# Kernel tuning notes

Measured on AMD Instinct MI355X. Metric: run time of the kernel, lower is better.

The kernel has to match this reference:

```python
import jax, jax.numpy as jnp
import numpy as np

K = 32  # neighbors, from init kwarg k


def setup_inputs() -> dict:
    key = jax.random.key(0)
    k1, k2, k3, k4 = jax.random.split(key, 4)
    N_train, N_test, D = 32768, 4096, 64
    x_train = jax.random.normal(k1, (N_train, D), dtype=jnp.float32)
    y_train = jax.random.randint(k2, (N_train,), 0, 1000, dtype=jnp.int64)
    x_test = jax.random.normal(k3, (N_test, D), dtype=jnp.float32)
    w_train = jax.random.uniform(k4, (N_train,), dtype=jnp.float32)
    return {"x_train": x_train, "y_train": y_train, "x_test": x_test, "w_train": w_train}


def _cdist(a, b):
    # Euclidean distance matrix [Na, Nb], matching torch.cdist(p=2)
    a2 = jnp.sum(a * a, axis=-1, keepdims=True)          # [Na,1]
    b2 = jnp.sum(b * b, axis=-1)[None, :]                # [1,Nb]
    sq = a2 + b2 - 2.0 * (a @ b.T)
    return jnp.sqrt(jnp.maximum(sq, 0.0))


def reference(x_train, y_train, x_test, w_train):
    n_test = x_test.shape[0]
    n_train = x_train.shape[0]
    dists = _cdist(x_test, x_train)                      # [N_test, N_train]
    # k smallest distances -> negate and take top_k
    _, indices = jax.lax.top_k(-dists, K)                # [N_test, K]
    knn_labels = y_train[indices]                        # [N_test, K]
    knn_w = w_train[indices]                             # [N_test, K]
    # weighted scatter vote: vote_pool[j, y_train[i]] += w_train[i]
    rows = jnp.arange(n_test)[:, None]                   # [N_test, 1]
    vote_pool = jnp.zeros((n_test, n_train), dtype=jnp.float32)
    vote_pool = vote_pool.at[rows, knn_labels].add(knn_w)
    return jnp.argmax(vote_pool, axis=1)
```

## Files before the change

kernel.cpp:

```cpp
#include <hip/hip_runtime.h>

#define NTRAIN 32768
#define NTEST  4096
#define DIM    64
#define KSEL   32
#define NLAB   1000
#define NCH    16
#define CHCOLS 2048
#define SLOT   112
#define NBIN   256
#define SSAMP  8192
#define SRANK2 32
#define POOLCAP 1792
#define WCOEF  0.01f

using short8 = __attribute__((ext_vector_type(8))) short;
using f32x4  = __attribute__((ext_vector_type(4))) float;
typedef unsigned short u16;

__device__ __forceinline__ unsigned f2u(float f){
  unsigned b = __float_as_uint(f);
  return (b & 0x80000000u) ? ~b : (b | 0x80000000u);
}
__device__ __forceinline__ u16 f2b(float x){
  unsigned u = __float_as_uint(x);
  return (u16)((u + 0x7fffu + ((u >> 16) & 1u)) >> 16);
}

struct Sel {
  unsigned hist[2048];
  unsigned wsum[4];
  unsigned sB, sLess, sU;
  int sNeed;
};

__device__ unsigned radix_select(const unsigned* __restrict__ keys, int n,
                                 unsigned rank, Sel* s, int t, int* needOut)
{
  const int lane = t & 63, wid = t >> 6;
  unsigned target = rank, pref = 0;
  for (int lev = 0; lev < 3; ++lev){
    const int nb    = (lev == 2) ? 1024 : 2048;
    const int shift = (lev == 0) ? 21 : (lev == 1 ? 10 : 0);
    for (int q = t; q < nb; q += 256) s->hist[q] = 0;
    __syncthreads();
    for (int i = t; i < n; i += 256){
      unsigned u = keys[i];
      bool ok = (lev == 0) ? true
              : (lev == 1) ? ((u >> 21) == pref)
                           : ((u >> 10) == pref);
      if (ok) atomicAdd(&s->hist[(u >> shift) & (unsigned)(nb - 1)], 1u);
    }
    __syncthreads();
    const int g = nb / 256;
    unsigned sl = 0;
#pragma unroll
    for (int k = 0; k < 8; ++k) if (k < g) sl += s->hist[t*g + k];
    unsigned x = sl;
#pragma unroll
    for (int ofs = 1; ofs < 64; ofs <<= 1){
      unsigned v = __shfl_up(x, (unsigned)ofs, 64);
      if (lane >= ofs) x += v;
    }
    if (lane == 63) s->wsum[wid] = x;
    __syncthreads();
    unsigned woff = 0;
#pragma unroll
    for (int w = 0; w < 4; ++w) if (w < wid) woff += s->wsum[w];
    unsigned incl = x + woff;
    unsigned excl = incl - sl;
    if (excl < target && target <= incl){
      unsigned cum = excl; int b = t*g;
      while (cum + s->hist[b] < target){ cum += s->hist[b]; ++b; }
      s->sB = (unsigned)b; s->sLess = cum;
    }
    __syncthreads();
    unsigned B = s->sB, cl = s->sLess;
    target -= cl;
    if      (lev == 0) pref = B;
    else if (lev == 1) pref = (pref << 11) | B;
    else if (t == 0){ s->sU = (pref << 10) | B; s->sNeed = (int)target; }
  }
  __syncthreads();
  *needOut = s->sNeed;
  return s->sU;
}

__device__ void select32(const unsigned* ku, const unsigned* ki, int n,
                         Sel* s, unsigned* tieI, unsigned* selI,
                         int* selCnt, int* tieCnt, int t)
{
  int need;
  unsigned ustar = radix_select(ku, n, KSEL, s, t, &need);
  if (t == 0){ *selCnt = 0; *tieCnt = 0; }
  __syncthreads();
  for (int i = t; i < n; i += 256){
    unsigned u = ku[i];
    if (u < ustar){ int p = atomicAdd(selCnt, 1); if (p < 40) selI[p] = ki[i]; }
    else if (u == ustar){ int p = atomicAdd(tieCnt, 1); if (p < 256) tieI[p] = ki[i]; }
  }
  __syncthreads();
  int nT = *tieCnt; if (nT > 256) nT = 256;
  if (t < nT){
    unsigned my = tieI[t]; int r = 0;
    for (int k = 0; k < nT; ++k) r += (tieI[k] < my) ? 1 : 0;
    if (r < need){ int p = atomicAdd(selCnt, 1); if (p < 40) selI[p] = my; }
  }
  __syncthreads();
}

__global__ void calib(int* __restrict__ MT, int* __restrict__ JT,
                      int* __restrict__ okf)
{
  const int l = threadIdx.x;
  const int v = l & 15;
  short8 av, onev, kv;
  u16 vb  = f2b((float)(v + 1));
  u16 one = (u16)0x3F80;
#pragma unroll
  for (int e = 0; e < 8; ++e){
    ((u16*)&av)[e]   = vb;
    ((u16*)&onev)[e] = one;
    ((u16*)&kv)[e]   = f2b((float)((l >> 4)*8 + e + 1));
  }
  f32x4 dA = {0,0,0,0}, dB = {0,0,0,0}, dK = {0,0,0,0};
  dA = __builtin_amdgcn_mfma_f32_16x16x32_bf16(av, onev, dA, 0,0,0);
  dB = __builtin_amdgcn_mfma_f32_16x16x32_bf16(onev, av, dB, 0,0,0);
  dK = __builtin_amdgcn_mfma_f32_16x16x32_bf16(kv, kv, dK, 0,0,0);
  bool ok = true;
#pragma unroll
  for (int e = 0; e < 4; ++e){
    int mi = (int)(dA[e]*(1.0f/32.0f) + 0.5f) - 1;
    int ji = (int)(dB[e]*(1.0f/32.0f) + 0.5f) - 1;
    if (mi < 0 || mi > 15 || dA[e] != 32.0f*(float)(mi+1)) ok = false;
    if (ji < 0 || ji > 15 || dB[e] != 32.0f*(float)(ji+1)) ok = false;
    if (dK[e] != 11440.0f) ok = false;
    MT[l*4 + e] = mi & 15;
    JT[l*4 + e] = ji & 15;
  }
  unsigned long long bal = __ballot(ok);
  if (l == 0) okf[0] = (bal == ~0ull) ? 1 : 0;
}

__global__ __launch_bounds__(256) void prep(const float* __restrict__ xtr,
        u16* __restrict__ xtr16, float* __restrict__ hb2,
        float* __restrict__ stats)
{
  int j = blockIdx.x*256 + threadIdx.x;
  const float4* rp = (const float4*)(xtr + (size_t)j*DIM);
  u16* orow = xtr16 + (size_t)j*DIM;
  float s = 0.f;
#pragma unroll
  for (int q = 0; q < 16; ++q){
    float4 w = rp[q];
    uint2 pk;
    pk.x = (unsigned)f2b(w.x) | ((unsigned)f2b(w.y) << 16);
    pk.y = (unsigned)f2b(w.z) | ((unsigned)f2b(w.w) << 16);
    *(uint2*)(orow + q*4) = pk;
    s = fmaf(w.x,w.x,s); s = fmaf(w.y,w.y,s);
    s = fmaf(w.z,w.z,s); s = fmaf(w.w,w.w,s);
  }
  float hs = 0.5f * s;
  hb2[j] = hs;
  float r0 = hs, r1 = hs*hs, r2 = s;
#pragma unroll
  for (int msk = 1; msk < 64; msk <<= 1){
    r0 += __shfl_xor(r0, msk, 64);
    r1 += __shfl_xor(r1, msk, 64);
    r2 = fmaxf(r2, __shfl_xor(r2, msk, 64));
  }
  if ((threadIdx.x & 63) == 0){
    atomicAdd(&stats[0], r0);
    atomicAdd(&stats[1], r1);
    atomicMax((unsigned*)&stats[2], __float_as_uint(r2));
  }
}

__global__ __launch_bounds__(256) void prepT(const float* __restrict__ xtst,
        u16* __restrict__ xtst16, const float* __restrict__ stats,
        float* __restrict__ loT, float* __restrict__ bsT, float* __restrict__ Wt)
{
  int m = blockIdx.x*256 + threadIdx.x;
  const float4* rp = (const float4*)(xtst + (size_t)m*DIM);
  u16* orow = xtst16 + (size_t)m*DIM;
  float s = 0.f;
#pragma unroll
  for (int q = 0; q < 16; ++q){
    float4 w = rp[q];
    uint2 pk;
    pk.x = (unsigned)f2b(w.x) | ((unsigned)f2b(w.y) << 16);
    pk.y = (unsigned)f2b(w.z) | ((unsigned)f2b(w.w) << 16);
    *(uint2*)(orow + q*4) = pk;
    s = fmaf(w.x,w.x,s); s = fmaf(w.y,w.y,s);
    s = fmaf(w.z,w.z,s); s = fmaf(w.w,w.w,s);
  }
  const float invN = 1.0f/(float)NTRAIN;
  float C   = stats[0]*invN;
  float var = fmaxf(stats[1]*invN - C*C, 0.f);
  float mb  = __uint_as_float(*(const unsigned*)&stats[2]);
  float sig = sqrtf(var + s) + 1e-6f;
  loT[m] = C - 12.f*sig;
  bsT[m] = 16.f/sig;
  Wt[m]  = WCOEF * sqrtf(s * mb);
}

__global__ __launch_bounds__(256) void sampleT(const u16* __restrict__ xtr16,
        const u16* __restrict__ xtst16, const float* __restrict__ hb2,
        const float* __restrict__ loT, const float* __restrict__ bsT,
        const float* __restrict__ Wt, const int* __restrict__ MT,
        const int* __restrict__ JT, const int* __restrict__ okf,
        float* __restrict__ TfB, float* __restrict__ thrFB)
{
  __shared__ unsigned histL[16*NBIN];
  __shared__ float hbS[SSAMP];

  const int t = threadIdx.x, lane = t & 63, w = t >> 6;
  const int m0 = blockIdx.x * 16;
  if (okf[0] == 0){
    if (t < 16){ TfB[m0+t] = 0.f; thrFB[m0+t] = -3.0e38f; }
    return;
  }
  const int oprow = lane & 15, kgrp = lane >> 4;

  for (int i = t; i < 16*NBIN; i += 256) histL[i] = 0;
  for (int i = t; i < SSAMP; i += 256) hbS[i] = hb2[i];

  int Ml[4], Jl[4];
#pragma unroll
  for (int e = 0; e < 4; ++e){ Ml[e] = MT[lane*4+e]; Jl[e] = JT[lane*4+e]; }

  const u16* ap = xtst16 + (size_t)(m0 + oprow)*DIM + kgrp*8;
  short8 a00 = *(const short8*)ap;
  short8 a01 = *(const short8*)(ap + 32);

  float lo0[4], bs0[4];
#pragma unroll
  for (int e = 0; e < 4; ++e){
    lo0[e] = loT[m0 + Ml[e]]; bs0[e] = bsT[m0 + Ml[e]];
  }
  __syncthreads();

  const int wcol = w*(SSAMP/4);
  const u16* bp = xtr16 + (size_t)(wcol + oprow)*DIM + kgrp*8;

#pragma unroll 2
  for (int jt = 0; jt < SSAMP/64; ++jt){
    short8 b0 = *(const short8*)bp;
    short8 b1 = *(const short8*)(bp + 32);
    f32x4 c0 = {0.f,0.f,0.f,0.f};
    c0 = __builtin_amdgcn_mfma_f32_16x16x32_bf16(a00, b0, c0, 0,0,0);
    c0 = __builtin_amdgcn_mfma_f32_16x16x32_bf16(a01, b1, c0, 0,0,0);
    const int jl = wcol + jt*16;
#pragma unroll
    for (int e = 0; e < 4; ++e){
      float h = hbS[jl + Jl[e]];
      float f = (h - c0[e] - lo0[e]) * bs0[e];
      if (f < 161.f){
        int b = (f < 0.f) ? 0 : (int)f;
        atomicAdd(&histL[Ml[e]*NBIN + b], 1u);
      }
    }
    bp += 16*DIM;
  }
  __syncthreads();
  if (t < 16){
    const unsigned* h = &histL[t*NBIN];
    unsigned cum = 0; int b = -1;
    for (int i = 0; i <= 160; ++i){
      cum += h[i];
      if (cum >= SRANK2){ b = i; break; }
    }
    int m = m0 + t;
    if (b < 0){ TfB[m] = 0.f; thrFB[m] = -3.0e38f; }
    else {
      float Te = loT[m] + (float)(b + 1) / bsT[m];
      float Wv = Wt[m];
      TfB[m]   = Te + 1.5f*Wv;
      thrFB[m] = Te + 2.5f*Wv;
    }
  }
}

__global__ __launch_bounds__(256) void knnA(const u16* __restrict__ xtr16,
        const u16* __restrict__ xtst16, const float* __restrict__ hb2,
        const float* __restrict__ thrFB, const int* __restrict__ MT,
        const int* __restrict__ JT, const int* __restrict__ okf,
        unsigned* __restrict__ cnt2, u16* __restrict__ cand)
{
  __shared__ float hbS[CHCOLS];
  __shared__ u16 lbuf[32][SLOT];
  __shared__ unsigned lcnt[32];

  const int t = threadIdx.x, lane = t & 63, w = t >> 6;
  const int jc = blockIdx.x & (NCH-1), mg = blockIdx.x >> 4;
  const int m0 = mg*32, col0 = jc*CHCOLS;

  if (okf[0] == 0){
    if (t < 32) cnt2[(size_t)jc*NTEST + m0 + t] = 0xFFFFFFFFu;
    return;
  }
  const int oprow = lane & 15, kgrp = lane >> 4;

  if (t < 32) lcnt[t] = 0;
  for (int i = t; i < CHCOLS; i += 256) hbS[i] = hb2[col0 + i];

  int Ml[4], Jl[4];
#pragma unroll
  for (int e = 0; e < 4; ++e){ Ml[e] = MT[lane*4+e]; Jl[e] = JT[lane*4+e]; }

  const u16* ap = xtst16 + (size_t)(m0 + oprow)*DIM + kgrp*8;
  short8 a00 = *(const short8*)ap;
  short8 a01 = *(const short8*)(ap + 32);
  short8 a10 = *(const short8*)(ap + 16*DIM);
  short8 a11 = *(const short8*)(ap + 16*DIM + 32);

  float th0[4], th1[4];
#pragma unroll
  for (int e = 0; e < 4; ++e){
    th0[e] = thrFB[m0 + Ml[e]];
    th1[e] = thrFB[m0 + 16 + Ml[e]];
  }
  float tm0 = fmaxf(fmaxf(th0[0],th0[1]), fmaxf(th0[2],th0[3]));
  float tm1 = fmaxf(fmaxf(th1[0],th1[1]), fmaxf(th1[2],th1[3]));

  __syncthreads();

  const int wcol = w*(CHCOLS/4);
  const u16* bp = xtr16 + (size_t)(col0 + wcol + oprow)*DIM + kgrp*8;

#pragma unroll 2
  for (int jt = 0; jt < CHCOLS/64; ++jt){
    short8 b0 = *(const short8*)bp;
    short8 b1 = *(const short8*)(bp + 32);
    f32x4 c0 = {0.f,0.f,0.f,0.f}, c1 = {0.f,0.f,0.f,0.f};
    c0 = __builtin_amdgcn_mfma_f32_16x16x32_bf16(a00, b0, c0, 0,0,0);
    c0 = __builtin_amdgcn_mfma_f32_16x16x32_bf16(a01, b1, c0, 0,0,0);
    c1 = __builtin_amdgcn_mfma_f32_16x16x32_bf16(a10, b0, c1, 0,0,0);
    c1 = __builtin_amdgcn_mfma_f32_16x16x32_bf16(a11, b1, c1, 0,0,0);
    const int jl = wcol + jt*16;
    float h[4];
#pragma unroll
    for (int e = 0; e < 4; ++e) h[e] = hbS[jl + Jl[e]];
    float g0 = fmaxf(fmaxf(c0[0]-h[0], c0[1]-h[1]), fmaxf(c0[2]-h[2], c0[3]-h[3]));
    if (g0 + tm0 > 0.f){
#pragma unroll
      for (int e = 0; e < 4; ++e) if (h[e] - c0[e] < th0[e]){
        unsigned p = atomicAdd(&lcnt[Ml[e]], 1u);
        if (p < SLOT) lbuf[Ml[e]][p] = (u16)(jl + Jl[e]);
      }
    }
    float g1 = fmaxf(fmaxf(c1[0]-h[0], c1[1]-h[1]), fmaxf(c1[2]-h[2], c1[3]-h[3]));
    if (g1 + tm1 > 0.f){
#pragma unroll
      for (int e = 0; e < 4; ++e) if (h[e] - c1[e] < th1[e]){
        unsigned p = atomicAdd(&lcnt[16 + Ml[e]], 1u);
        if (p < SLOT) lbuf[16 + Ml[e]][p] = (u16)(jl + Jl[e]);
      }
    }
    bp += 16*DIM;
  }
  __syncthreads();
  if (t < 32) cnt2[(size_t)jc*NTEST + m0 + t] = lcnt[t];
  const unsigned* lb32 = (const unsigned*)lbuf;
  unsigned* c32 = (unsigned*)cand;
  for (int i = t; i < 32*(SLOT/2); i += 256){
    int ms = i / (SLOT/2), e = i - ms*(SLOT/2);
    c32[((size_t)(m0 + ms)*NCH + jc)*(SLOT/2) + e] = lb32[i];
  }
}

__global__ __launch_bounds__(256) void knnB(const float* __restrict__ x_train,
        const float* __restrict__ hb2, const float* __restrict__ x_test,
        const int* __restrict__ y_train, const float* __restrict__ w_train,
        const float* __restrict__ TfB, const int* __restrict__ okf,
        const unsigned* __restrict__ cnt2, const u16* __restrict__ cand,
        int* __restrict__ out)
{
  __shared__ unsigned ku[POOLCAP], ki[POOLCAP];
  __shared__ unsigned chunkKeys[1024];
  __shared__ Sel ss;
  __shared__ unsigned tieI[256];
  __shared__ unsigned selI[40];
  __shared__ unsigned selR[KSEL];
  __shared__ int selCnt, tieCnt, poolCnt, nBelow, badJ;
  __shared__ float votes[NLAB];
  __shared__ unsigned cntS[NCH];
  __shared__ int yv[KSEL]; __shared__ float wv[KSEL];

  const int t = threadIdx.x, m = blockIdx.x;
  float a[DIM];
  const float4* am = (const float4*)(x_test + (size_t)m*DIM);
#pragma unroll
  for (int q = 0; q < 16; ++q){
    float4 v = am[q];
    a[4*q]=v.x; a[4*q+1]=v.y; a[4*q+2]=v.z; a[4*q+3]=v.w;
  }
  if (t < NCH) cntS[t] = cnt2[(size_t)t*NTEST + m];
  if (t == 0){ nBelow = 0; badJ = 0; }
  __syncthreads();

  bool ovf = (okf[0] == 0);
  unsigned offs[NCH+1]; offs[0] = 0;
#pragma unroll
  for (int jcc = 0; jcc < NCH; ++jcc){
    unsigned cc = cntS[jcc];
    if (cc > SLOT) ovf = true;
    offs[jcc+1] = offs[jcc] + ((cc > SLOT) ? SLOT : cc);
  }
  int c = (int)offs[NCH];
  bool mainok = !ovf && c >= KSEL;

  if (mainok){
#pragma unroll
    for (int jcc = 0; jcc < NCH; ++jcc){
      unsigned cc = cntS[jcc];
      for (unsigned i = t; i < cc; i += 256){
        unsigned v = cand[((size_t)m*NCH + jcc)*SLOT + i];
        if (v >= CHCOLS){ badJ = 1; v = 0; }
        ki[offs[jcc] + i] = (unsigned)(jcc*CHCOLS) + v;
      }
    }
    __syncthreads();
    if (badJ) mainok = false;
  }
  const float Tf = TfB[m];
  if (mainok){
    for (int i = t; i < c; i += 256){
      unsigned j = ki[i];
      const float4* rp = (const float4*)(x_train + (size_t)j*DIM);
      float s = 0.f;
#pragma unroll
      for (int q = 0; q < 16; ++q){
        float4 v = rp[q];
        s = fmaf(a[4*q],v.x,s); s = fmaf(a[4*q+1],v.y,s);
        s = fmaf(a[4*q+2],v.z,s); s = fmaf(a[4*q+3],v.w,s);
      }
      float kf = hb2[j] - s;
      ku[i] = f2u(kf);
      if (kf < Tf) atomicAdd(&nBelow, 1);
    }
    __syncthreads();
    mainok = (nBelow >= KSEL);
  }

  if (mainok){
    select32(ku, ki, c, &ss, tieI, selI, &selCnt, &tieCnt, t);
    if (t < KSEL) selR[t] = selI[t];
    __syncthreads();
  } else {
    if (t == 0) poolCnt = 0;
    __syncthreads();
    for (int ch = 0; ch < NTRAIN/1024; ++ch){
      const int j0 = ch*1024;
      for (int q = 0; q < 4; ++q){
        int j = j0 + q*256 + t;
        const float4* rp = (const float4*)(x_train + (size_t)j*DIM);
        float s = 0.f;
#pragma unroll
        for (int qq = 0; qq < 16; ++qq){
          float4 v = rp[qq];
          s = fmaf(a[4*qq],v.x,s); s = fmaf(a[4*qq+1],v.y,s);
          s = fmaf(a[4*qq+2],v.z,s); s = fmaf(a[4*qq+3],v.w,s);
        }
        chunkKeys[q*256 + t] = f2u(hb2[j] - s);
      }
      __syncthreads();
      int need;
      unsigned ustar = radix_select(chunkKeys, 1024, KSEL, &ss, t, &need);
      for (int q = 0; q < 4; ++q){
        unsigned u = chunkKeys[q*256 + t];
        if (u <= ustar){
          int p = atomicAdd(&poolCnt, 1);
          if (p < POOLCAP){ ku[p] = u; ki[p] = (unsigned)(j0 + q*256 + t); }
        }
      }
      __syncthreads();
    }
    int n = poolCnt; if (n > POOLCAP) n = POOLCAP;
    select32(ku, ki, n, &ss, tieI, selI, &selCnt, &tieCnt, t);
    if (t < KSEL) selR[t] = selI[t];
    __syncthreads();
  }

  for (int q = t; q < NLAB; q += 256) votes[q] = 0.f;
  if (t < KSEL){
    unsigned my = selR[t]; int r = 0;
#pragma unroll
    for (int k = 0; k < KSEL; ++k) r += (selR[k] < my) ? 1 : 0;
    yv[r] = y_train[my]; wv[r] = w_train[my];
  }
  __syncthreads();
  if (t == 0){
    for (int r = 0; r < KSEL; ++r) votes[yv[r]] += wv[r];
  }
  __syncthreads();

  float* rv = (float*)ss.hist;
  int*   rl = (int*)(ss.hist + 256);
  float bv = -1.f; int bl = 0;
  for (int l = t; l < NLAB; l += 256){
    float v = votes[l];
    if (v > bv){ bv = v; bl = l; }
  }
  rv[t] = bv; rl[t] = bl;
  __syncthreads();
  for (int sred = 128; sred > 0; sred >>= 1){
    if (t < sred){
      if (rv[t+sred] > rv[t] || (rv[t+sred] == rv[t] && rl[t+sred] < rl[t])){
        rv[t] = rv[t+sred]; rl[t] = rl[t+sred];
      }
    }
    __syncthreads();
  }
  if (t == 0) out[m] = rl[0];
}

__global__ __launch_bounds__(256) void knn_legacy(
    const float* __restrict__ x_train, const float* __restrict__ x_test,
    const int* __restrict__ y_train, const float* __restrict__ w_train,
    int* __restrict__ out)
{
  __shared__ unsigned keys[16384];
  __shared__ Sel ss;
  __shared__ unsigned candU[64];
  __shared__ unsigned candI[64];
  __shared__ unsigned tieI[256];
  __shared__ int nCand, nTie;
  __shared__ float rv[256]; __shared__ int rl[256];

  float* votes = (float*)ss.hist;
  const int t = threadIdx.x;
  const int m = blockIdx.x;

  float a[DIM];
  const float* am = x_test + (size_t)m * DIM;
#pragma unroll
  for (int d = 0; d < DIM; ++d) a[d] = am[d];

  if (t == 0) nCand = 0;

  for (int h = 0; h < 2; ++h){
    __syncthreads();
    for (int i = 0; i < 64; ++i){
      int j = h*16384 + i*256 + t;
      const float4* bp = (const float4*)(x_train + (size_t)j * DIM);
      float s = 0.f;
#pragma unroll
      for (int q = 0; q < 16; ++q){
        float4 v = bp[q];
        float e0 = a[4*q]   - v.x, e1 = a[4*q+1] - v.y;
        float e2 = a[4*q+2] - v.z, e3 = a[4*q+3] - v.w;
        s = fmaf(e0,e0,s); s = fmaf(e1,e1,s); s = fmaf(e2,e2,s); s = fmaf(e3,e3,s);
      }
      keys[i*256 + t] = f2u(s);
    }
    __syncthreads();

    int need;
    unsigned ustar = radix_select(keys, 16384, KSEL, &ss, t, &need);
    if (t == 0) nTie = 0;
    __syncthreads();

    for (int i = 0; i < 64; ++i){
      unsigned u   = keys[i*256 + t];
      unsigned idx = (unsigned)(h*16384 + i*256 + t);
      if (u < ustar){
        int p = atomicAdd(&nCand, 1);
        if (p < 64){ candU[p] = u; candI[p] = idx; }
      } else if (u == ustar){
        int p = atomicAdd(&nTie, 1);
        if (p < 256) tieI[p] = idx;
      }
    }
    __syncthreads();
    int nT = nTie; if (nT > 256) nT = 256;
    if (t < nT){
      unsigned my = tieI[t]; int r = 0;
      for (int k = 0; k < nT; ++k) r += (tieI[k] < my) ? 1 : 0;
      if (r < need){
        int p = atomicAdd(&nCand, 1);
        if (p < 64){ candU[p] = ustar; candI[p] = my; }
      }
    }
    __syncthreads();
  }

  for (int q = t; q < NLAB; q += 256) votes[q] = 0.f;
  __syncthreads();
  int nC = nCand; if (nC > 64) nC = 64;
  if (t < nC){
    unsigned mu = candU[t], mi = candI[t];
    int r = 0;
    for (int k = 0; k < nC; ++k){
      unsigned kku = candU[k], kki = candI[k];
      r += (kku < mu || (kku == mu && kki < mi)) ? 1 : 0;
    }
    if (r < KSEL){
      int lab = y_train[mi];
      atomicAdd(&votes[lab], w_train[mi]);
    }
  }
  __syncthreads();

  float bv = -1.f; int bl = 0;
  for (int l = t; l < NLAB; l += 256){
    float v = votes[l];
    if (v > bv){ bv = v; bl = l; }
  }
  rv[t] = bv; rl[t] = bl;
  __syncthreads();
  for (int s = 128; s > 0; s >>= 1){
    if (t < s){
      if (rv[t+s] > rv[t] || (rv[t+s] == rv[t] && rl[t+s] < rl[t])){
        rv[t] = rv[t+s]; rl[t] = rl[t+s];
      }
    }
    __syncthreads();
  }
  if (t == 0) out[m] = rl[0];
}

extern "C" void kernel_launch(void* const* d_in, const int* in_sizes, int n_in,
                              void* d_out, int out_size, void* d_ws, size_t ws_size,
                              hipStream_t stream)
{
  (void)in_sizes; (void)n_in; (void)out_size;
  const float* x_train = (const float*)d_in[0];
  const int*   y_train = (const int*)  d_in[1];
  const float* x_test  = (const float*)d_in[2];
  const float* w_train = (const float*)d_in[3];
  int* out = (int*)d_out;

  char* p = (char*)d_ws;
  u16*      xtr16  = (u16*)p;      p += (size_t)NTRAIN*DIM*2;
  u16*      xtst16 = (u16*)p;      p += (size_t)NTEST*DIM*2;
  float*    hb2    = (float*)p;    p += (size_t)NTRAIN*4;
  float*    loT    = (float*)p;    p += (size_t)NTEST*4;
  float*    bsT    = (float*)p;    p += (size_t)NTEST*4;
  float*    Wt     = (float*)p;    p += (size_t)NTEST*4;
  float*    TfB    = (float*)p;    p += (size_t)NTEST*4;
  float*    thrFB  = (float*)p;    p += (size_t)NTEST*4;
  unsigned* cnt2   = (unsigned*)p; p += (size_t)NCH*NTEST*4;
  int*      MT     = (int*)p;      p += 64*4*4;
  int*      JT     = (int*)p;      p += 64*4*4;
  int*      okf    = (int*)p;      p += 256;
  float*    stats  = (float*)p;    p += 512;
  u16*      cand   = (u16*)p;      p += (size_t)NTEST*NCH*SLOT*2;
  size_t need = (size_t)(p - (char*)d_ws);

  if (ws_size >= need){
    hipMemsetAsync(stats, 0, 512, stream);
    calib<<<1, 64, 0, stream>>>(MT, JT, okf);
    prep <<<NTRAIN/256, 256, 0, stream>>>(x_train, xtr16, hb2, stats);
    prepT<<<NTEST/256,  256, 0, stream>>>(x_test, xtst16, stats, loT, bsT, Wt);
    sampleT<<<NTEST/16, 256, 0, stream>>>(xtr16, xtst16, hb2, loT, bsT, Wt,
                                          MT, JT, okf, TfB, thrFB);
    knnA<<<(NTEST/32)*NCH, 256, 0, stream>>>(xtr16, xtst16, hb2, thrFB,
                                             MT, JT, okf, cnt2, cand);
    knnB<<<NTEST, 256, 0, stream>>>(x_train, hb2, x_test, y_train, w_train,
                                    TfB, okf, cnt2, cand, out);
  } else {
    knn_legacy<<<NTEST, 256, 0, stream>>>(x_train, x_test, y_train, w_train, out);
  }
}
```

Baseline: 304.3 us.

## Split threshold sampling across blocks, compact knnB candidates and shrink shared memory

The sampleT histogram pass is split into two half-sample blocks per row group. Each block merges its local histogram into a global histogram with atomics, and a new scanT kernel derives the thresholds from it. In knnB, only candidates below the threshold are compacted into a small buffer and ranked directly, which replaces the general radix select32 on the main path. Shared arrays are overlaid in a union to cut LDS use, and the final argmax uses wave shuffles instead of a shared-memory tree. The cost is an extra kernel launch, a memset, global atomics, and an O(n²) rank step that depends on how many candidates fall below the threshold.

```diff
diff --git a/kernel.cpp b/kernel.cpp
--- a/kernel.cpp
+++ b/kernel.cpp
@@ -10,7 +10,9 @@
 #define SLOT   112
 #define NBIN   256
 #define SSAMP  8192
+#define SHALF  (SSAMP/2)
 #define SRANK2 32
+#define SCAP   512
 #define POOLCAP 1792
 #define WCOEF  0.01f
 
@@ -207,23 +209,20 @@
 __global__ __launch_bounds__(256) void sampleT(const u16* __restrict__ xtr16,
         const u16* __restrict__ xtst16, const float* __restrict__ hb2,
         const float* __restrict__ loT, const float* __restrict__ bsT,
-        const float* __restrict__ Wt, const int* __restrict__ MT,
-        const int* __restrict__ JT, const int* __restrict__ okf,
-        float* __restrict__ TfB, float* __restrict__ thrFB)
+        const int* __restrict__ MT, const int* __restrict__ JT,
+        const int* __restrict__ okf, unsigned* __restrict__ ghist)
 {
   __shared__ unsigned histL[16*NBIN];
-  __shared__ float hbS[SSAMP];
-
+  __shared__ float hbS[SHALF];
+
+  if (okf[0] == 0) return;
   const int t = threadIdx.x, lane = t & 63, w = t >> 6;
-  const int m0 = blockIdx.x * 16;
-  if (okf[0] == 0){
-    if (t < 16){ TfB[m0+t] = 0.f; thrFB[m0+t] = -3.0e38f; }
-    return;
-  }
+  const int g = blockIdx.x >> 1, half = blockIdx.x & 1;
+  const int m0 = g * 16, row0 = half * SHALF;
   const int oprow = lane & 15, kgrp = lane >> 4;
 
   for (int i = t; i < 16*NBIN; i += 256) histL[i] = 0;
-  for (int i = t; i < SSAMP; i += 256) hbS[i] = hb2[i];
+  for (int i = t; i < SHALF; i += 256) hbS[i] = hb2[row0 + i];
 
   int Ml[4], Jl[4];
 #pragma unroll
@@ -240,11 +239,11 @@
   }
   __syncthreads();
 
-  const int wcol = w*(SSAMP/4);
-  const u16* bp = xtr16 + (size_t)(wcol + oprow)*DIM + kgrp*8;
+  const int wcol = w*(SHALF/4);
+  const u16* bp = xtr16 + (size_t)(row0 + wcol + oprow)*DIM + kgrp*8;
 
 #pragma unroll 2
-  for (int jt = 0; jt < SSAMP/64; ++jt){
+  for (int jt = 0; jt < SHALF/64; ++jt){
     short8 b0 = *(const short8*)bp;
     short8 b1 = *(const short8*)(bp + 32);
     f32x4 c0 = {0.f,0.f,0.f,0.f};
@@ -263,21 +262,33 @@
     bp += 16*DIM;
   }
   __syncthreads();
-  if (t < 16){
-    const unsigned* h = &histL[t*NBIN];
-    unsigned cum = 0; int b = -1;
-    for (int i = 0; i <= 160; ++i){
-      cum += h[i];
-      if (cum >= SRANK2){ b = i; break; }
-    }
-    int m = m0 + t;
-    if (b < 0){ TfB[m] = 0.f; thrFB[m] = -3.0e38f; }
-    else {
-      float Te = loT[m] + (float)(b + 1) / bsT[m];
-      float Wv = Wt[m];
-      TfB[m]   = Te + 1.5f*Wv;
-      thrFB[m] = Te + 2.5f*Wv;
-    }
+  for (int i = t; i < 16*NBIN; i += 256){
+    unsigned v = histL[i];
+    if (v) atomicAdd(&ghist[(size_t)(m0 + (i >> 8))*NBIN + (i & 255)], v);
+  }
+}
+
+__global__ __launch_bounds__(256) void scanT(const unsigned* __restrict__ ghist,
+        const float* __restrict__ loT, const float* __restrict__ bsT,
+        const float* __restrict__ Wt, float* __restrict__ TfB,
+        float* __restrict__ thrFB)
+{
+  int m = blockIdx.x*256 + threadIdx.x;
+  const uint4* h4 = (const uint4*)(ghist + (size_t)m*NBIN);
+  unsigned cum = 0; int b = -1;
+  for (int i4 = 0; i4 < 41 && b < 0; ++i4){
+    uint4 v = h4[i4];
+    unsigned c0 = cum + v.x, c1 = c0 + v.y, c2 = c1 + v.z, c3 = c2 + v.w;
+    if (c3 >= SRANK2)
+      b = i4*4 + ((c0 >= SRANK2) ? 0 : (c1 >= SRANK2) ? 1 : (c2 >= SRANK2) ? 2 : 3);
+    cum = c3;
+  }
+  if (b < 0){ TfB[m] = 0.f; thrFB[m] = -3.0e38f; }
+  else {
+    float Te = loT[m] + (float)(b + 1) / bsT[m];
+    float Wv = Wt[m];
+    TfB[m]   = Te + 1.5f*Wv;
+    thrFB[m] = Te + 2.5f*Wv;
   }
 }
 
@@ -376,16 +387,17 @@
         const unsigned* __restrict__ cnt2, const u16* __restrict__ cand,
         int* __restrict__ out)
 {
-  __shared__ unsigned ku[POOLCAP], ki[POOLCAP];
-  __shared__ unsigned chunkKeys[1024];
-  __shared__ Sel ss;
-  __shared__ unsigned tieI[256];
-  __shared__ unsigned selI[40];
+  __shared__ unsigned cntS[NCH];
   __shared__ unsigned selR[KSEL];
-  __shared__ int selCnt, tieCnt, poolCnt, nBelow, badJ;
-  __shared__ float votes[NLAB];
-  __shared__ unsigned cntS[NCH];
   __shared__ int yv[KSEL]; __shared__ float wv[KSEL];
+  __shared__ int nBelow, badJ, poolCnt, selCnt, tieCnt;
+  __shared__ float wrv[4]; __shared__ int wrl[4];
+  __shared__ union {
+    struct { unsigned ki[NCH*SLOT]; unsigned bu[SCAP]; unsigned bi[SCAP]; } mp;
+    struct { unsigned ku[POOLCAP]; unsigned ki[POOLCAP]; unsigned ck[1024];
+             Sel ss; unsigned tieI[256]; unsigned selI[40]; } fb;
+    struct { float votes[NLAB]; } vt;
+  } u;
 
   const int t = threadIdx.x, m = blockIdx.x;
   float a[DIM];
@@ -417,16 +429,16 @@
       for (unsigned i = t; i < cc; i += 256){
         unsigned v = cand[((size_t)m*NCH + jcc)*SLOT + i];
         if (v >= CHCOLS){ badJ = 1; v = 0; }
-        ki[offs[jcc] + i] = (unsigned)(jcc*CHCOLS) + v;
+        u.mp.ki[offs[jcc] + i] = (unsigned)(jcc*CHCOLS) + v;
       }
     }
     __syncthreads();
     if (badJ) mainok = false;
   }
-  const float Tf = TfB[m];
+  const unsigned Tfu = f2u(TfB[m]);
   if (mainok){
     for (int i = t; i < c; i += 256){
-      unsigned j = ki[i];
+      unsigned j = u.mp.ki[i];
       const float4* rp = (const float4*)(x_train + (size_t)j*DIM);
       float s = 0.f;
 #pragma unroll
@@ -435,17 +447,27 @@
         s = fmaf(a[4*q],v.x,s); s = fmaf(a[4*q+1],v.y,s);
         s = fmaf(a[4*q+2],v.z,s); s = fmaf(a[4*q+3],v.w,s);
       }
-      float kf = hb2[j] - s;
-      ku[i] = f2u(kf);
-      if (kf < Tf) atomicAdd(&nBelow, 1);
-    }
-    __syncthreads();
-    mainok = (nBelow >= KSEL);
+      unsigned ku = f2u(hb2[j] - s);
+      if (ku < Tfu){
+        int p = atomicAdd(&nBelow, 1);
+        if (p < SCAP){ u.mp.bu[p] = ku; u.mp.bi[p] = j; }
+      }
+    }
+    __syncthreads();
+    mainok = (nBelow >= KSEL && nBelow <= SCAP);
   }
 
   if (mainok){
-    select32(ku, ki, c, &ss, tieI, selI, &selCnt, &tieCnt, t);
-    if (t < KSEL) selR[t] = selI[t];
+    int ns = nBelow;
+    for (int i = t; i < ns; i += 256){
+      unsigned mu = u.mp.bu[i], mi = u.mp.bi[i];
+      int r = 0;
+      for (int k = 0; k < ns; ++k){
+        unsigned kk = u.mp.bu[k], kj = u.mp.bi[k];
+        r += (kk < mu || (kk == mu && kj < mi)) ? 1 : 0;
+      }
+      if (r < KSEL) selR[r] = mi;
+    }
     __syncthreads();
   } else {
     if (t == 0) poolCnt = 0;
@@ -462,27 +484,28 @@
           s = fmaf(a[4*qq],v.x,s); s = fmaf(a[4*qq+1],v.y,s);
           s = fmaf(a[4*qq+2],v.z,s); s = fmaf(a[4*qq+3],v.w,s);
         }
-        chunkKeys[q*256 + t] = f2u(hb2[j] - s);
+        u.fb.ck[q*256 + t] = f2u(hb2[j] - s);
       }
       __syncthreads();
       int need;
-      unsigned ustar = radix_select(chunkKeys, 1024, KSEL, &ss, t, &need);
+      unsigned ustar = radix_select(u.fb.ck, 1024, KSEL, &u.fb.ss, t, &need);
       for (int q = 0; q < 4; ++q){
-        unsigned u = chunkKeys[q*256 + t];
-        if (u <= ustar){
+        unsigned uu = u.fb.ck[q*256 + t];
+        if (uu <= ustar){
           int p = atomicAdd(&poolCnt, 1);
-          if (p < POOLCAP){ ku[p] = u; ki[p] = (unsigned)(j0 + q*256 + t); }
+          if (p < POOLCAP){ u.fb.ku[p] = uu; u.fb.ki[p] = (unsigned)(j0 + q*256 + t); }
         }
       }
       __syncthreads();
     }
     int n = poolCnt; if (n > POOLCAP) n = POOLCAP;
-    select32(ku, ki, n, &ss, tieI, selI, &selCnt, &tieCnt, t);
-    if (t < KSEL) selR[t] = selI[t];
-    __syncthreads();
-  }
-
-  for (int q = t; q < NLAB; q += 256) votes[q] = 0.f;
+    select32(u.fb.ku, u.fb.ki, n, &u.fb.ss, u.fb.tieI, u.fb.selI,
+             &selCnt, &tieCnt, t);
+    if (t < KSEL) selR[t] = u.fb.selI[t];
+    __syncthreads();
+  }
+
+  for (int q = t; q < NLAB; q += 256) u.vt.votes[q] = 0.f;
   if (t < KSEL){
     unsigned my = selR[t]; int r = 0;
 #pragma unroll
@@ -491,28 +514,30 @@
   }
   __syncthreads();
   if (t == 0){
-    for (int r = 0; r < KSEL; ++r) votes[yv[r]] += wv[r];
-  }
-  __syncthreads();
-
-  float* rv = (float*)ss.hist;
-  int*   rl = (int*)(ss.hist + 256);
+    for (int r = 0; r < KSEL; ++r) u.vt.votes[yv[r]] += wv[r];
+  }
+  __syncthreads();
+
   float bv = -1.f; int bl = 0;
   for (int l = t; l < NLAB; l += 256){
-    float v = votes[l];
+    float v = u.vt.votes[l];
     if (v > bv){ bv = v; bl = l; }
   }
-  rv[t] = bv; rl[t] = bl;
-  __syncthreads();
-  for (int sred = 128; sred > 0; sred >>= 1){
-    if (t < sred){
-      if (rv[t+sred] > rv[t] || (rv[t+sred] == rv[t] && rl[t+sred] < rl[t])){
-        rv[t] = rv[t+sred]; rl[t] = rl[t+sred];
-      }
-    }
-    __syncthreads();
-  }
-  if (t == 0) out[m] = rl[0];
+#pragma unroll
+  for (int ofs = 1; ofs < 64; ofs <<= 1){
+    float ov = __shfl_xor(bv, ofs, 64);
+    int   ol = __shfl_xor(bl, ofs, 64);
+    if (ov > bv || (ov == bv && ol < bl)){ bv = ov; bl = ol; }
+  }
+  if ((t & 63) == 0){ wrv[t >> 6] = bv; wrl[t >> 6] = bl; }
+  __syncthreads();
+  if (t == 0){
+#pragma unroll
+    for (int w = 1; w < 4; ++w){
+      if (wrv[w] > bv || (wrv[w] == bv && wrl[w] < bl)){ bv = wrv[w]; bl = wrl[w]; }
+    }
+    out[m] = bl;
+  }
 }
 
 __global__ __launch_bounds__(256) void knn_legacy(
@@ -648,13 +673,17 @@
   u16*      cand   = (u16*)p;      p += (size_t)NTEST*NCH*SLOT*2;
   size_t need = (size_t)(p - (char*)d_ws);
 
+  unsigned* ghist = (unsigned*)cand;
+
   if (ws_size >= need){
     hipMemsetAsync(stats, 0, 512, stream);
+    hipMemsetAsync(ghist, 0, (size_t)NTEST*NBIN*4, stream);
     calib<<<1, 64, 0, stream>>>(MT, JT, okf);
     prep <<<NTRAIN/256, 256, 0, stream>>>(x_train, xtr16, hb2, stats);
     prepT<<<NTEST/256,  256, 0, stream>>>(x_test, xtst16, stats, loT, bsT, Wt);
-    sampleT<<<NTEST/16, 256, 0, stream>>>(xtr16, xtst16, hb2, loT, bsT, Wt,
-                                          MT, JT, okf, TfB, thrFB);
+    sampleT<<<(NTEST/16)*2, 256, 0, stream>>>(xtr16, xtst16, hb2, loT, bsT,
+                                              MT, JT, okf, ghist);
+    scanT<<<NTEST/256, 256, 0, stream>>>(ghist, loT, bsT, Wt, TfB, thrFB);
     knnA<<<(NTEST/32)*NCH, 256, 0, stream>>>(xtr16, xtst16, hb2, thrFB,
                                              MT, JT, okf, cnt2, cand);
     knnB<<<NTEST, 256, 0, stream>>>(x_train, hb2, x_test, y_train, w_train,
```

Result: slower. 466.8 us (+53.4%).
